# Optimization experiments

Measured on AMD Instinct MI355X. Metric: run time of the kernel, lower is better.

Reference implementation:

```python
import jax, jax.numpy as jnp
from jax import lax
import numpy as np

B, CIN, COUT, T, H, W, KH, KW = 8, 256, 256, 16, 28, 28, 3, 3


def setup_inputs() -> dict:
    key = jax.random.key(0)
    k1, k2, k3 = jax.random.split(key, 3)
    x = jax.random.normal(k1, (B, CIN, T, H, W), dtype=jnp.float32)
    alpha = jax.random.uniform(k2, (B, CIN, T, 1, 1), dtype=jnp.float32)
    # base weight, kaiming-uniform-like init, stored as [1,1,c_out,c_in,kh,kw]
    fan_in = CIN * KH * KW
    bound = 1.0 / np.sqrt(fan_in)
    weight = jax.random.uniform(k3, (1, 1, COUT, CIN, KH, KW), dtype=jnp.float32,
                                minval=-bound, maxval=bound)
    return {"x": x, "alpha": alpha, "weight": weight}


def reference(x, alpha, weight):
    # x: [b, c_in, t, h, w]; alpha: [b, c_in, t, 1, 1]; weight: [1,1,c_out,c_in,kh,kw]
    b, c_in, t, h, w = x.shape
    c_out = weight.shape[2]
    w_base = weight[0, 0]  # [c_out, c_in, kh, kw]
    # W_t = alpha_t * W_base scales only input channels (alpha broadcasts over c_out),
    # so (alpha*W) conv x == W conv (alpha*x): modulate input, then one shared conv.
    xm = x * alpha  # [b, c_in, t, h, w]
    xm = jnp.transpose(xm, (0, 2, 1, 3, 4)).reshape(b * t, c_in, h, w)
    y = lax.conv_general_dilated(
        xm, w_base,
        window_strides=(1, 1),
        padding=((1, 1), (1, 1)),
        dimension_numbers=("NCHW", "OIHW", "NCHW"),
    )  # [b*t, c_out, h, w]
    oh, ow = y.shape[-2], y.shape[-1]
    y = y.reshape(b, t, c_out, oh, ow)
    return jnp.transpose(y, (0, 2, 1, 3, 4))  # [b, c_out, t, h, w]
```

## Files before the change

kernel.cpp:

```cpp
#include <hip/hip_runtime.h>
#include <hip/hip_bf16.h>
#include <cstdint>

#define CIN   256
#define COUT  256
#define NB    8
#define NT    16
#define NH    28
#define NW    28
#define HP    30
#define WP    30

#define XM_ELEMS   ((size_t)NB * NT * HP * WP * CIN)
#define XM_BYTES   (XM_ELEMS * 2)

typedef __bf16 bf16x8 __attribute__((ext_vector_type(8)));
typedef float  f32x4  __attribute__((ext_vector_type(4)));

#define AS1 __attribute__((address_space(1)))
#define AS3 __attribute__((address_space(3)))

static __device__ __forceinline__ unsigned short f2bf(float f) {
    __hip_bfloat16 h = __float2bfloat16(f);
    return __builtin_bit_cast(unsigned short, h);
}

__global__ void modulate_kernel(const float* __restrict__ x,
                                const float* __restrict__ alpha,
                                unsigned short* __restrict__ xm) {
    const int ci = threadIdx.x;
    const int blk = blockIdx.x;
    const int hp = blk % 30;
    const int bt = blk / 30;
    unsigned short* row = xm + (size_t)(bt * 900 + hp * 30) * 256;
    if (hp == 0 || hp == 29) {
        #pragma unroll
        for (int wp = 0; wp < 30; ++wp) row[wp * 256 + ci] = 0;
        return;
    }
    const int t = bt & 15, b = bt >> 4;
    const int h = hp - 1;
    const float a = alpha[(b * CIN + ci) * NT + t];
    const float* xrow = x + ((size_t)((b * CIN + ci) * NT + t) * NH + h) * NW;
    row[ci] = 0;
    row[29 * 256 + ci] = 0;
    const float4* xv = (const float4*)xrow;
    #pragma unroll
    for (int q = 0; q < 7; ++q) {
        float4 v = xv[q];
        row[(q * 4 + 1) * 256 + ci] = f2bf(v.x * a);
        row[(q * 4 + 2) * 256 + ci] = f2bf(v.y * a);
        row[(q * 4 + 3) * 256 + ci] = f2bf(v.z * a);
        row[(q * 4 + 4) * 256 + ci] = f2bf(v.w * a);
    }
}

__global__ void repack_w_kernel(const float* __restrict__ w,
                                unsigned short* __restrict__ wB) {
    const int ci = threadIdx.x;
    const int tap = blockIdx.x >> 8;
    const int co  = blockIdx.x & 255;
    wB[((tap * 256 + co) * 256) + ci] = f2bf(w[(co * 256 + ci) * 9 + tap]);
}


#define BAR()    __builtin_amdgcn_s_barrier()
#define LGKM0()  asm volatile("s_waitcnt lgkmcnt(0)" ::: "memory")
#define VMW(N)   asm volatile("s_waitcnt vmcnt(" #N ")" ::: "memory")
#define SCHED0() __builtin_amdgcn_sched_barrier(0)

#define STAGE_F(P) do {                                                       \
    const int kh2 = (tapS * 11) >> 5;                                         \
    const int kw2 = tapS - 3 * kh2;                                           \
    const int aOff = tapS * 65536 + cicS * 32;                                \
    const int bOff = ((kh2 - 1) * 30 + (kw2 - 1)) * 256 + cicS * 32;          \
    _Pragma("unroll") for (int c_ = 0; c_ < 2; ++c_)                          \
        __builtin_amdgcn_global_load_lds(                                     \
            (const AS1 void*)(aSrc + aOff + c_ * 32768),                      \
            (AS3 void*)(lds + (P)*32768 + (c_*128 + wave*16)*64 + lane*16),   \
            16, 0, 0);                                                        \
    _Pragma("unroll") for (int c_ = 0; c_ < 2; ++c_)                          \
        __builtin_amdgcn_global_load_lds(                                     \
            (const AS1 void*)(bL[c_] + bOff),                                 \
            (AS3 void*)(lds + (P)*32768 + 16384 + (c_*128 + wave*16)*64 + lane*16), \
            16, 0, 0);                                                        \
    if (++tapS == 9) { tapS = 0; ++cicS; }                                    \
} while (0)

#define READF(S, P) do {                                                      \
    _Pragma("unroll") for (int m_ = 0; m_ < 4; ++m_)                          \
        fa##S[m_] = *(const bf16x8*)(lds + (P)*32768 +                        \
            (wm*64 + m_*16 + l15)*64 + readSwz);                              \
    _Pragma("unroll") for (int f_ = 0; f_ < NF; ++f_)                         \
        fb##S[f_] = *(const bf16x8*)(lds + (P)*32768 + 16384 +                \
            (wn*(NF*16) + f_*16 + l15)*64 + readSwz);                         \
} while (0)

#define MFMA_T(S) do {                                                        \
    _Pragma("unroll") for (int m_ = 0; m_ < 4; ++m_)                          \
    _Pragma("unroll") for (int f_ = 0; f_ < NF; ++f_)                         \
        acc[m_][f_] = __builtin_amdgcn_mfma_f32_16x16x32_bf16(                \
            fb##S[f_], fa##S[m_], acc[m_][f_], 0, 0, 0);                      \
} while (0)

#define BODY_S(CS, NS, NBUF, SBUF) do {                                       \
    VMW(4);                                                                   \
    SCHED0();                                                                 \
    BAR();                                                                    \
    READF(NS, NBUF);                                                          \
    STAGE_F(SBUF);                                                            \
    SCHED0();                                                                 \
    MFMA_T(CS);                                                               \
    LGKM0();                                                                  \
    SCHED0();                                                                 \
} while (0)

#define BODY_N(CS, NS, NBUF, VMN) do {                                        \
    VMW(VMN);                                                                 \
    SCHED0();                                                                 \
    BAR();                                                                    \
    READF(NS, NBUF);                                                          \
    SCHED0();                                                                 \
    MFMA_T(CS);                                                               \
    LGKM0();                                                                  \
    SCHED0();                                                                 \
} while (0)

template<int NF>
__device__ __forceinline__ void conv_body(
    const unsigned short* __restrict__ xm,
    const unsigned short* __restrict__ wB,
    float* __restrict__ out,
    char* lds, const int n0)
{
    const int tid  = threadIdx.x;
    const int wave = tid >> 6;
    const int lane = tid & 63;
    const int l15  = lane & 15;
    const int wm   = wave >> 1;
    const int wn   = wave & 1;
    const int BN   = NF * 32;

    const int swzE = 8 * ((lane & 3) ^ ((lane >> 3) & 3));
    const unsigned short* aSrc = wB + (wave * 16 + (lane >> 2)) * 256 + swzE;

    const unsigned short* bL[2];
    #pragma unroll
    for (int c_ = 0; c_ < 2; ++c_) {
        int nl = c_ * 128 + wave * 16 + (lane >> 2);
        nl = nl > BN - 1 ? BN - 1 : nl;
        const int n  = n0 + nl;
        const int w_ = n % 28, h_ = (n / 28) % 28, bt = n / 784;
        bL[c_] = xm + (size_t)((bt * 30 + h_ + 1) * 30 + (w_ + 1)) * 256 + swzE;
    }

    const int readSwz = ((lane >> 4) ^ ((l15 >> 1) & 3)) << 4;

    f32x4 acc[4][NF];
    #pragma unroll
    for (int i = 0; i < 4; ++i)
        #pragma unroll
        for (int j = 0; j < NF; ++j) acc[i][j] = f32x4{0.f, 0.f, 0.f, 0.f};

    bf16x8 faA[4], fbA[NF], faB[4], fbB[NF];

    int tapS = 0, cicS = 0;
    STAGE_F(0);
    STAGE_F(1);
    STAGE_F(2);
    VMW(8);
    SCHED0();
    BAR();
    READF(A, 0);
    LGKM0();
    SCHED0();

    #pragma unroll 1
    for (int it = 0; it < 11; ++it) {
        BODY_S(A, B, 1, 0);
        BODY_S(B, A, 2, 1);
        BODY_S(A, B, 0, 2);
        BODY_S(B, A, 1, 0);
        BODY_S(A, B, 2, 1);
        BODY_S(B, A, 0, 2);
    }
    BODY_S(A, B, 1, 0);
    BODY_S(B, A, 2, 1);
    BODY_S(A, B, 0, 2);
    BODY_N(B, A, 1, 4);
    BODY_N(A, B, 2, 0);
    MFMA_T(B);

    #pragma unroll
    for (int f = 0; f < NF; ++f) {
        const int n  = n0 + wn * (NF * 16) + f * 16 + ((lane >> 4) << 2);
        const int bt = n / 784;
        const int hw = n - bt * 784;
        const int b = bt >> 4, t = bt & 15;
        float* obase = out + ((size_t)(b * 256) * 16 + t) * 784 + hw;
        #pragma unroll
        for (int m = 0; m < 4; ++m) {
            const int co = wm * 64 + m * 16 + l15;
            *(f32x4*)(obase + (size_t)co * 12544) = acc[m][f];
        }
    }
}

__global__ __launch_bounds__(512, 2) void conv_gemm_kernel(
    const unsigned short* __restrict__ xm,
    const unsigned short* __restrict__ wB,
    float* __restrict__ out) {
    __shared__ __align__(1024) char lds[98304];
    const int bx = blockIdx.x;
    if (bx < 64) {
        conv_body<7>(xm, wB, out, lds, bx * 224);
    } else {
        conv_body<6>(xm, wB, out, lds, 14336 + (bx - 64) * 192);
    }
}

extern "C" void kernel_launch(void* const* d_in, const int* in_sizes, int n_in,
                              void* d_out, int out_size, void* d_ws, size_t ws_size,
                              hipStream_t stream) {
    const float* x      = (const float*)d_in[0];
    const float* alpha  = (const float*)d_in[1];
    const float* weight = (const float*)d_in[2];
    float* out = (float*)d_out;

    unsigned short* xm = (unsigned short*)d_ws;
    unsigned short* wB = (unsigned short*)((char*)d_ws + XM_BYTES);

    modulate_kernel<<<dim3(NB * NT * HP), dim3(256), 0, stream>>>(x, alpha, xm);
    repack_w_kernel<<<dim3(9 * 256), dim3(256), 0, stream>>>(weight, wB);
    conv_gemm_kernel<<<dim3(512), dim3(512), 0, stream>>>(xm, wB, out);
}
```

Before: 157.1 us.

## Load weight fragments directly to registers and deepen activation LDS pipeline

```diff
diff --git a/kernel.cpp b/kernel.cpp
--- a/kernel.cpp
+++ b/kernel.cpp
@@ -69,30 +69,28 @@
 #define VMW(N)   asm volatile("s_waitcnt vmcnt(" #N ")" ::: "memory")
 #define SCHED0() __builtin_amdgcn_sched_barrier(0)
 
-#define STAGE_F(P) do {                                                       \
+#define STAGE_B(P) do {                                                       \
     const int kh2 = (tapS * 11) >> 5;                                         \
     const int kw2 = tapS - 3 * kh2;                                           \
-    const int aOff = tapS * 65536 + cicS * 32;                                \
     const int bOff = ((kh2 - 1) * 30 + (kw2 - 1)) * 256 + cicS * 32;          \
     _Pragma("unroll") for (int c_ = 0; c_ < 2; ++c_)                          \
         __builtin_amdgcn_global_load_lds(                                     \
-            (const AS1 void*)(aSrc + aOff + c_ * 32768),                      \
-            (AS3 void*)(lds + (P)*32768 + (c_*128 + wave*16)*64 + lane*16),   \
-            16, 0, 0);                                                        \
-    _Pragma("unroll") for (int c_ = 0; c_ < 2; ++c_)                          \
-        __builtin_amdgcn_global_load_lds(                                     \
             (const AS1 void*)(bL[c_] + bOff),                                 \
-            (AS3 void*)(lds + (P)*32768 + 16384 + (c_*128 + wave*16)*64 + lane*16), \
+            (AS3 void*)(lds + (P)*16384 + (c_*128 + wave*16)*64 + lane*16),   \
             16, 0, 0);                                                        \
     if (++tapS == 9) { tapS = 0; ++cicS; }                                    \
 } while (0)
 
-#define READF(S, P) do {                                                      \
+#define LOADA(S) do {                                                         \
+    const unsigned short* ap_ = aRow + tapA * 65536 + cicA * 32;              \
     _Pragma("unroll") for (int m_ = 0; m_ < 4; ++m_)                          \
-        fa##S[m_] = *(const bf16x8*)(lds + (P)*32768 +                        \
-            (wm*64 + m_*16 + l15)*64 + readSwz);                              \
+        fa##S[m_] = *(const bf16x8*)(ap_ + m_ * 4096);                        \
+    if (++tapA == 9) { tapA = 0; ++cicA; }                                    \
+} while (0)
+
+#define READF_B(S, P) do {                                                    \
     _Pragma("unroll") for (int f_ = 0; f_ < NF; ++f_)                         \
-        fb##S[f_] = *(const bf16x8*)(lds + (P)*32768 + 16384 +                \
+        fb##S[f_] = *(const bf16x8*)(lds + (P)*16384 +                        \
             (wn*(NF*16) + f_*16 + l15)*64 + readSwz);                         \
 } while (0)
 
@@ -103,25 +101,27 @@
             fb##S[f_], fa##S[m_], acc[m_][f_], 0, 0, 0);                      \
 } while (0)
 
-#define BODY_S(CS, NS, NBUF, SBUF) do {                                       \
-    VMW(4);                                                                   \
+#define BODY_F(CS, NS, NBUF, SBUF) do {                                       \
+    VMW(6);                                                                   \
     SCHED0();                                                                 \
     BAR();                                                                    \
-    READF(NS, NBUF);                                                          \
-    STAGE_F(SBUF);                                                            \
+    READF_B(NS, NBUF);                                                        \
+    STAGE_B(SBUF);                                                            \
     SCHED0();                                                                 \
     MFMA_T(CS);                                                               \
+    LOADA(CS);                                                                \
     LGKM0();                                                                  \
     SCHED0();                                                                 \
 } while (0)
 
-#define BODY_N(CS, NS, NBUF, VMN) do {                                        \
+#define BODY_T(CS, NS, NBUF, VMN, DO_LOADA) do {                              \
     VMW(VMN);                                                                 \
     SCHED0();                                                                 \
     BAR();                                                                    \
-    READF(NS, NBUF);                                                          \
+    READF_B(NS, NBUF);                                                        \
     SCHED0();                                                                 \
     MFMA_T(CS);                                                               \
+    if (DO_LOADA) LOADA(CS);                                                  \
     LGKM0();                                                                  \
     SCHED0();                                                                 \
 } while (0)
@@ -141,9 +141,10 @@
     const int wn   = wave & 1;
     const int BN   = NF * 32;
 
+    const unsigned short* aRow =
+        wB + (wm * 64 + l15) * 256 + (lane >> 4) * 8;
+
     const int swzE = 8 * ((lane & 3) ^ ((lane >> 3) & 3));
-    const unsigned short* aSrc = wB + (wave * 16 + (lane >> 2)) * 256 + swzE;
-
     const unsigned short* bL[2];
     #pragma unroll
     for (int c_ = 0; c_ < 2; ++c_) {
@@ -162,33 +163,36 @@
         #pragma unroll
         for (int j = 0; j < NF; ++j) acc[i][j] = f32x4{0.f, 0.f, 0.f, 0.f};
 
-    bf16x8 faA[4], fbA[NF], faB[4], fbB[NF];
+    bf16x8 faA[4], faB[4], fbA[NF], fbB[NF];
 
     int tapS = 0, cicS = 0;
-    STAGE_F(0);
-    STAGE_F(1);
-    STAGE_F(2);
-    VMW(8);
+    int tapA = 0, cicA = 0;
+
+    STAGE_B(0);
+    STAGE_B(1);
+    STAGE_B(2);
+    STAGE_B(3);
+    LOADA(A);
+    LOADA(B);
+    VMW(4);
     SCHED0();
     BAR();
-    READF(A, 0);
+    READF_B(A, 0);
     LGKM0();
     SCHED0();
 
     #pragma unroll 1
-    for (int it = 0; it < 11; ++it) {
-        BODY_S(A, B, 1, 0);
-        BODY_S(B, A, 2, 1);
-        BODY_S(A, B, 0, 2);
-        BODY_S(B, A, 1, 0);
-        BODY_S(A, B, 2, 1);
-        BODY_S(B, A, 0, 2);
-    }
-    BODY_S(A, B, 1, 0);
-    BODY_S(B, A, 2, 1);
-    BODY_S(A, B, 0, 2);
-    BODY_N(B, A, 1, 4);
-    BODY_N(A, B, 2, 0);
+    for (int it = 0; it < 17; ++it) {
+        BODY_F(A, B, 1, 0);
+        BODY_F(B, A, 2, 1);
+        BODY_F(A, B, 3, 2);
+        BODY_F(B, A, 0, 3);
+    }
+    BODY_T(A, B, 1, 6, true);
+    BODY_T(B, A, 2, 4, true);
+    BODY_T(A, B, 3, 4, false);
+    VMW(0);
+    SCHED0();
     MFMA_T(B);
 
     #pragma unroll
@@ -210,7 +214,7 @@
     const unsigned short* __restrict__ xm,
     const unsigned short* __restrict__ wB,
     float* __restrict__ out) {
-    __shared__ __align__(1024) char lds[98304];
+    __shared__ __align__(1024) char lds[65536];
     const int bx = blockIdx.x;
     if (bx < 64) {
         conv_body<7>(xm, wB, out, lds, bx * 224);
```

New measurement: 224.0 us. 42.6% more time.
